# Optimization experiments

Measured on AMD Instinct MI355X. Metric: run time of the kernel, lower is better.

Reference implementation:

```python
import jax, jax.numpy as jnp
import numpy as np

C = 512

def _conv1x1(x, w, b):
    # x: [B, C, T], w: [O, C], b: [O] -> [B, O, T]
    return jnp.einsum('oc,bct->bot', w, x) + b[None, :, None]

def setup_inputs() -> dict:
    key = jax.random.key(0)
    ks = jax.random.split(key, 9)
    B, T = 8, 2048
    s = 1.0 / np.sqrt(C)
    inp = {'x': jax.random.normal(ks[0], (B, C, T), dtype=jnp.float32)}
    names = ['theta', 'phi', 'g', 'w']
    for i, n in enumerate(names):
        inp[f'w_{n}'] = jax.random.uniform(ks[1 + 2 * i], (C, C), jnp.float32, -s, s)
        inp[f'b_{n}'] = jax.random.uniform(ks[2 + 2 * i], (C,), jnp.float32, -s, s)
    return inp

def reference(x, w_theta, b_theta, w_phi, b_phi, w_g, b_g, w_w, b_w):
    relu = jax.nn.relu
    feat_theta = relu(_conv1x1(x, w_theta, b_theta))          # [B, C, T]
    feat_phi = relu(_conv1x1(x, w_phi, b_phi))                # [B, C, T]
    # scores: Q^T K over channel dim -> [B, T, T]
    scores = jnp.einsum('bci,bcj->bij', feat_theta, feat_phi)
    attn = jax.nn.softmax(scores, axis=2)                     # [B, T, T]
    feat_g = relu(_conv1x1(x, w_g, b_g))                      # [B, C, T]
    # attention-weighted V: [B, T, T] x [B, T, C] -> [B, T, C] -> [B, C, T]
    feature = jnp.einsum('bij,bcj->bci', attn, feat_g)
    w_feature = relu(_conv1x1(feature, w_w, b_w))
    return w_feature + x
```

## Files before the change

### kernel.cpp

```cpp
#include <hip/hip_runtime.h>
#include <math.h>

#define C_DIM 512
#define T_DIM 2048
#define B_DIM 8

typedef _Float16 f16;
typedef __attribute__((ext_vector_type(8))) _Float16 half8;
typedef __attribute__((ext_vector_type(4))) _Float16 half4;
typedef __attribute__((ext_vector_type(4))) float floatx4;

__global__ __launch_bounds__(256) void prep_kernel(
    const float* __restrict__ x, f16* __restrict__ xt,
    const float* __restrict__ w0, const float* __restrict__ w1,
    const float* __restrict__ w2, const float* __restrict__ w3,
    f16* __restrict__ o0, f16* __restrict__ o1,
    f16* __restrict__ o2, f16* __restrict__ o3,
    const float* __restrict__ b0, const float* __restrict__ b1,
    float* __restrict__ ob)
{
    __shared__ float xs[32][33];
    const int blk = blockIdx.x;
    const int tid = threadIdx.x;

    if (blk < 1024) {
        const float* src; f16* dst;
        switch (blk >> 8) {
            case 0:  src = w0; dst = o0; break;
            case 1:  src = w1; dst = o1; break;
            case 2:  src = w2; dst = o2; break;
            default: src = w3; dst = o3; break;
        }
        const int idx = ((blk & 255) * 256 + tid) * 4;
        const float4 v = *(const float4*)(src + idx);
        half4 h; h[0] = (f16)v.x; h[1] = (f16)v.y; h[2] = (f16)v.z; h[3] = (f16)v.w;
        *(half4*)(dst + idx) = h;
        return;
    }
    if (blk < 1028) {
        const int i = (blk - 1024) * 256 + tid;
        ob[i] = (i < 512) ? b0[i] : b1[i - 512];
        return;
    }
    {
        const int rr = blk - 1028;
        const int b  = rr >> 10;
        const int rem = rr & 1023;
        const int t0 = (rem & 63) * 32;
        const int c0 = (rem >> 6) * 32;
        const float* xb = x + (size_t)b * C_DIM * T_DIM;
        const int r = tid >> 3, q = tid & 7;

        const float4 v = *(const float4*)(xb + (size_t)(c0 + r) * T_DIM + t0 + q * 4);
        xs[r][q * 4 + 0] = v.x; xs[r][q * 4 + 1] = v.y;
        xs[r][q * 4 + 2] = v.z; xs[r][q * 4 + 3] = v.w;
        __syncthreads();

        f16* xtb = xt + (size_t)b * C_DIM * T_DIM;
        half4 h;
        h[0] = (f16)xs[q * 4 + 0][r]; h[1] = (f16)xs[q * 4 + 1][r];
        h[2] = (f16)xs[q * 4 + 2][r]; h[3] = (f16)xs[q * 4 + 3][r];
        *(half4*)(xtb + (size_t)(t0 + r) * C_DIM + c0 + q * 4) = h;
    }
}

__device__ __forceinline__ void gl16(const f16* g, f16* l)
{
    __builtin_amdgcn_global_load_lds(
        (const __attribute__((address_space(1))) unsigned int*)g,
        (__attribute__((address_space(3))) unsigned int*)l,
        16, 0, 0);
}


template<int MODE>
__global__ __launch_bounds__(512, 2) void gemm256(
    const f16* __restrict__ A, size_t sA, int lda,
    const f16* __restrict__ B, size_t sB, int ldb,
    void* __restrict__ Cp, size_t sC, int ldc,
    const float* __restrict__ bias,
    int gx, int K)
{
    __shared__ __align__(16) f16 As[2][2][256 * 32];
    __shared__ __align__(16) f16 Bs[2][2][256 * 32];

    const int f = blockIdx.x;
    const int bz = f & 7;
    const int flat = f >> 3;
    const int jsc = gx >> 2;
    const int sh = (jsc <= 1) ? 0 : (31 - __builtin_clz(jsc));
    const int s = flat >> 4, rem = flat & 15;
    const int i0 = ((s >> sh) * 4 + (rem >> 2)) * 256;
    const int j0 = (((jsc <= 1) ? 0 : (s & (jsc - 1))) * 4 + (rem & 3)) * 256;

    A += (size_t)bz * sA;
    B += (size_t)bz * sB;

    const int tid  = threadIdx.x;
    const int lane = tid & 63;
    const int wave = tid >> 6;
    const int wy = wave >> 2;
    const int wx = wave & 3;
    const int quad = lane >> 4, l16 = lane & 15;

    const int srow = wave * 32 + (lane >> 2);
    const int sch  = (lane & 3) ^ ((lane >> 3) & 3);
    const f16* gA0 = A + (size_t)(i0 + srow) * lda + sch * 8;
    const f16* gA1 = gA0 + (size_t)16 * lda;
    const f16* gB0 = B + (size_t)(j0 + srow) * ldb + sch * 8;
    const f16* gB1 = gB0 + (size_t)16 * ldb;
    const int wsg = wave * 1024;

    const int xq = (quad ^ ((l16 >> 1) & 3)) << 3;
    const int ra = (wy * 128 + l16) * 32 + xq;
    const int rb = (wx * 64 + l16) * 32 + xq;

    const int nt = K >> 6;

#define STAGE_A(t, q) do {                                                    \
        const int off_ = (t) * 64 + (q) * 32;                                 \
        gl16(gA0 + off_, &As[(t) & 1][q][wsg]);                               \
        gl16(gA1 + off_, &As[(t) & 1][q][wsg + 512]);                         \
    } while (0)
#define STAGE_B(t, q) do {                                                    \
        const int off_ = (t) * 64 + (q) * 32;                                 \
        gl16(gB0 + off_, &Bs[(t) & 1][q][wsg]);                               \
        gl16(gB1 + off_, &Bs[(t) & 1][q][wsg + 512]);                         \
    } while (0)
#define PH_MFMA(B0) do {                                                      \
        __builtin_amdgcn_s_setprio(1);                                        \
        _Pragma("unroll")                                                     \
        for (int mi = 0; mi < 4; ++mi) {                                      \
            _Pragma("unroll")                                                 \
            for (int ni = 0; ni < 4; ++ni)                                    \
                acc[(B0) + mi][ni] = __builtin_amdgcn_mfma_f32_16x16x32_f16(  \
                    af[mi], bf[ni], acc[(B0) + mi][ni], 0, 0, 0);             \
        }                                                                     \
        __builtin_amdgcn_s_setprio(0);                                        \
    } while (0)

    STAGE_A(0, 0); STAGE_B(0, 0);
    STAGE_A(0, 1); STAGE_B(0, 1);
    STAGE_A(1, 0); STAGE_B(1, 0);

    floatx4 acc[8][4] = {};

    for (int t = 0; t < nt; ++t) {
        const f16* sa0 = &As[t & 1][0][0];
        const f16* sb0 = &Bs[t & 1][0][0];
        const f16* sa1 = &As[t & 1][1][0];
        const f16* sb1 = &Bs[t & 1][1][0];
        half8 af[4], bf[4];

        if (t + 1 < nt) asm volatile("s_waitcnt vmcnt(8)\ns_barrier" ::: "memory");
        else            asm volatile("s_waitcnt vmcnt(4)\ns_barrier" ::: "memory");
        #pragma unroll
        for (int ni = 0; ni < 4; ++ni) bf[ni] = *(const half8*)&sb0[rb + ni * 512];
        #pragma unroll
        for (int mi = 0; mi < 4; ++mi) af[mi] = *(const half8*)&sa0[ra + mi * 512];
        if (t + 1 < nt) STAGE_A(t + 1, 1);
        PH_MFMA(0);

        #pragma unroll
        for (int mi = 0; mi < 4; ++mi) af[mi] = *(const half8*)&sa0[ra + 2048 + mi * 512];
        if (t + 1 < nt) STAGE_B(t + 1, 1);
        PH_MFMA(4);

        if (t + 1 < nt) asm volatile("s_waitcnt vmcnt(8)\ns_barrier" ::: "memory");
        else            asm volatile("s_waitcnt vmcnt(0)\ns_barrier" ::: "memory");
        #pragma unroll
        for (int ni = 0; ni < 4; ++ni) bf[ni] = *(const half8*)&sb1[rb + ni * 512];
        #pragma unroll
        for (int mi = 0; mi < 4; ++mi) af[mi] = *(const half8*)&sa1[ra + mi * 512];
        if (t + 2 < nt) STAGE_A(t + 2, 0);
        PH_MFMA(0);

        #pragma unroll
        for (int mi = 0; mi < 4; ++mi) af[mi] = *(const half8*)&sa1[ra + 2048 + mi * 512];
        if (t + 2 < nt) STAGE_B(t + 2, 0);
        PH_MFMA(4);
    }
#undef STAGE_A
#undef STAGE_B
#undef PH_MFMA

    #pragma unroll
    for (int m = 0; m < 8; ++m) {
        #pragma unroll
        for (int ni = 0; ni < 4; ++ni) {
            const int col = j0 + wx * 64 + ni * 16 + l16;
            #pragma unroll
            for (int r = 0; r < 4; ++r) {
                const int row = i0 + wy * 128 + m * 16 + quad * 4 + r;
                float v = acc[m][ni][r];
                if (MODE == 1) { v += bias[col]; v = v > 0.f ? v : 0.f; }
                ((f16*)Cp)[(size_t)bz * sC + (size_t)row * ldc + col] = (f16)v;
            }
        }
    }
}

template<int MODE>
__global__ __launch_bounds__(512, 2) void gemm_wide(
    const f16* __restrict__ A, size_t sA, int lda,
    const f16* __restrict__ B, size_t sB, int ldb,
    void* __restrict__ Cp, size_t sC, int ldc,
    const float* __restrict__ bias,
    const float* __restrict__ resid, size_t sR,
    int gxn, int K)
{
    __shared__ __align__(16) f16 As[2][2][128 * 32];
    __shared__ __align__(16) f16 Bs[2][2][256 * 32];

    const int f = blockIdx.x;
    const int bz = f & 7;
    const int inner = f >> 3;
    const int j0 = (inner % gxn) * 256;
    const int i0 = (inner / gxn) * 128;
    A += (size_t)bz * sA;
    B += (size_t)bz * sB;

    const int tid  = threadIdx.x;
    const int lane = tid & 63;
    const int wave = tid >> 6;
    const int wy = wave >> 2;
    const int wx = wave & 3;
    const int quad = lane >> 4, l16 = lane & 15;

    const int sch = (lane & 3) ^ ((lane >> 3) & 3);
    const f16* gA0 = A + (size_t)(i0 + wave * 16 + (lane >> 2)) * lda + sch * 8;
    const f16* gB0 = B + (size_t)(j0 + wave * 32 + (lane >> 2)) * ldb + sch * 8;
    const f16* gB1 = gB0 + (size_t)16 * ldb;

    const int xq = (quad ^ ((l16 >> 1) & 3)) << 3;
    const int ra = (wy * 64 + l16) * 32 + xq;
    const int rb = (wx * 64 + l16) * 32 + xq;

    const int nt = K >> 6;

#define WSTAGE_A(t, q) do {                                                   \
        gl16(gA0 + (t) * 64 + (q) * 32, &As[(t) & 1][q][wave * 512]);         \
    } while (0)
#define WSTAGE_B(t, q) do {                                                   \
        const int off_ = (t) * 64 + (q) * 32;                                 \
        gl16(gB0 + off_, &Bs[(t) & 1][q][wave * 1024]);                       \
        gl16(gB1 + off_, &Bs[(t) & 1][q][wave * 1024 + 512]);                 \
    } while (0)
#define WPH_MFMA() do {                                                       \
        __builtin_amdgcn_s_setprio(1);                                        \
        _Pragma("unroll")                                                     \
        for (int mi = 0; mi < 4; ++mi) {                                      \
            _Pragma("unroll")                                                 \
            for (int ni = 0; ni < 4; ++ni)                                    \
                acc[mi][ni] = __builtin_amdgcn_mfma_f32_16x16x32_f16(         \
                    af[mi], bf[ni], acc[mi][ni], 0, 0, 0);                    \
        }                                                                     \
        __builtin_amdgcn_s_setprio(0);                                        \
    } while (0)

    WSTAGE_A(0, 0); WSTAGE_B(0, 0);
    WSTAGE_A(0, 1); WSTAGE_B(0, 1);
    WSTAGE_A(1, 0); WSTAGE_B(1, 0);

    floatx4 acc[4][4] = {};

    for (int t = 0; t < nt; ++t) {
        const f16* sa0 = &As[t & 1][0][0];
        const f16* sb0 = &Bs[t & 1][0][0];
        const f16* sa1 = &As[t & 1][1][0];
        const f16* sb1 = &Bs[t & 1][1][0];
        half8 af[4], bf[4];

        if (t + 1 < nt) asm volatile("s_waitcnt vmcnt(6)\ns_barrier" ::: "memory");
        else            asm volatile("s_waitcnt vmcnt(3)\ns_barrier" ::: "memory");
        #pragma unroll
        for (int ni = 0; ni < 4; ++ni) bf[ni] = *(const half8*)&sb0[rb + ni * 512];
        #pragma unroll
        for (int mi = 0; mi < 4; ++mi) af[mi] = *(const half8*)&sa0[ra + mi * 512];
        if (t + 1 < nt) { WSTAGE_A(t + 1, 1); WSTAGE_B(t + 1, 1); }
        WPH_MFMA();

        if (t + 1 < nt) asm volatile("s_waitcnt vmcnt(6)\ns_barrier" ::: "memory");
        else            asm volatile("s_waitcnt vmcnt(0)\ns_barrier" ::: "memory");
        #pragma unroll
        for (int ni = 0; ni < 4; ++ni) bf[ni] = *(const half8*)&sb1[rb + ni * 512];
        #pragma unroll
        for (int mi = 0; mi < 4; ++mi) af[mi] = *(const half8*)&sa1[ra + mi * 512];
        if (t + 2 < nt) { WSTAGE_A(t + 2, 0); WSTAGE_B(t + 2, 0); }
        WPH_MFMA();
    }
#undef WSTAGE_A
#undef WSTAGE_B
#undef WPH_MFMA

    #pragma unroll
    for (int mi = 0; mi < 4; ++mi) {
        #pragma unroll
        for (int ni = 0; ni < 4; ++ni) {
            const int col = j0 + wx * 64 + ni * 16 + l16;
            #pragma unroll
            for (int r = 0; r < 4; ++r) {
                const int row = i0 + wy * 64 + mi * 16 + quad * 4 + r;
                float v = acc[mi][ni][r];
                if (MODE == 2) { v += bias[row]; v = v > 0.f ? v : 0.f; }
                if (MODE == 3) {
                    v += bias[row];
                    v = v > 0.f ? v : 0.f;
                    v += resid[(size_t)bz * sR + (size_t)row * ldc + col];
                    ((float*)Cp)[(size_t)bz * sC + (size_t)row * ldc + col] = v;
                } else {
                    ((f16*)Cp)[(size_t)bz * sC + (size_t)row * ldc + col] = (f16)v;
                }
            }
        }
    }
}

__global__ __launch_bounds__(256) void softmax_f16_kernel(f16* __restrict__ S)
{
    const int lane = threadIdx.x & 63;
    f16* p = S + (size_t)(blockIdx.x * 4 + (threadIdx.x >> 6)) * T_DIM;

    half8 h[4];
    float v[32];
    float m = -1e30f;
    #pragma unroll
    for (int u = 0; u < 4; ++u) {
        h[u] = *((const half8*)p + (u * 64 + lane));
        #pragma unroll
        for (int c = 0; c < 8; ++c) {
            v[u * 8 + c] = (float)h[u][c];
            m = fmaxf(m, v[u * 8 + c]);
        }
    }
    #pragma unroll
    for (int off = 32; off; off >>= 1) m = fmaxf(m, __shfl_xor(m, off));

    float s = 0.f;
    #pragma unroll
    for (int i = 0; i < 32; ++i) { v[i] = __expf(v[i] - m); s += v[i]; }
    #pragma unroll
    for (int off = 32; off; off >>= 1) s += __shfl_xor(s, off);
    const float inv = 1.f / s;

    #pragma unroll
    for (int u = 0; u < 4; ++u) {
        #pragma unroll
        for (int c = 0; c < 8; ++c) h[u][c] = (f16)(v[u * 8 + c] * inv);
        *((half8*)p + (u * 64 + lane)) = h[u];
    }
}

extern "C" void kernel_launch(void* const* d_in, const int* in_sizes, int n_in,
                              void* d_out, int out_size, void* d_ws, size_t ws_size,
                              hipStream_t stream)
{
    const float* x       = (const float*)d_in[0];
    const float* w_theta = (const float*)d_in[1];
    const float* b_theta = (const float*)d_in[2];
    const float* w_phi   = (const float*)d_in[3];
    const float* b_phi   = (const float*)d_in[4];
    const float* w_g     = (const float*)d_in[5];
    const float* b_g     = (const float*)d_in[6];
    const float* w_w     = (const float*)d_in[7];
    const float* b_w     = (const float*)d_in[8];
    float* out = (float*)d_out;

    const size_t FE = (size_t)B_DIM * C_DIM * T_DIM;
    const size_t TC = (size_t)T_DIM * C_DIM;
    const size_t TT = (size_t)T_DIM * T_DIM;

    f16* xt      = (f16*)d_ws;
    f16* wtp     = xt + FE;
    f16* wg_h    = wtp + 524288;
    f16* ww_h    = wg_h + 262144;
    float* btp   = (float*)(ww_h + 262144);
    f16* tp      = (f16*)(btp + 1024);
    f16* g       = tp + (size_t)B_DIM * T_DIM * 1024;
    f16* scores  = g + FE;
    f16* feature = tp;

    const dim3 blk(256);
    const dim3 blk512(512);

    prep_kernel<<<dim3(1024 + 4 + 8192), blk, 0, stream>>>(
        x, xt, w_theta, w_phi, w_g, w_w,
        wtp, wtp + 262144, wg_h, ww_h, b_theta, b_phi, btp);

    gemm256<1><<<dim3(4 * 8 * B_DIM), blk512, 0, stream>>>(
        xt, TC, C_DIM, wtp, 0, C_DIM, tp, (size_t)T_DIM * 1024, 1024,
        btp, 4, C_DIM);
    gemm_wide<2><<<dim3(8 * 4 * B_DIM), blk512, 0, stream>>>(
        wg_h, 0, C_DIM, xt, TC, C_DIM, g, TC, T_DIM, b_g, nullptr, 0,
        8, C_DIM);
    gemm256<0><<<dim3(8 * 8 * B_DIM), blk512, 0, stream>>>(
        tp, (size_t)T_DIM * 1024, 1024, tp + 512, (size_t)T_DIM * 1024, 1024,
        scores, TT, T_DIM, nullptr, 8, C_DIM);
    softmax_f16_kernel<<<dim3(B_DIM * T_DIM / 4), blk, 0, stream>>>(scores);
    gemm_wide<0><<<dim3(2 * 16 * B_DIM), blk512, 0, stream>>>(
        scores, TT, T_DIM, g, TC, T_DIM, feature, TC, C_DIM,
        nullptr, nullptr, 0, 2, T_DIM);
    gemm_wide<3><<<dim3(8 * 4 * B_DIM), blk512, 0, stream>>>(
        ww_h, 0, C_DIM, feature, TC, C_DIM, out, TC, T_DIM, b_w, x, TC,
        8, C_DIM);
}
```

Baseline: 252.3 us.

## Compute two adjacent score tiles per block reusing A rows across tiles

Replaces the scores GEMM with a dual-tile kernel in which each block computes a 256x512 output strip as two consecutive 256x256 tiles, sweeping K twice. The pipelined loads continue straight into the second tile, so there is no separate prologue, and the first tile's accumulators are written out mid-loop. Grid size drops from 512 to 256 blocks, which cuts launch and prologue overhead and keeps the pipeline full across tiles. The cost is fewer blocks for occupancy and a write-out stall in the middle of the K loop.

```diff
diff --git a/kernel.cpp b/kernel.cpp
--- a/kernel.cpp
+++ b/kernel.cpp
@@ -198,6 +198,135 @@
             }
         }
     }
+}
+
+__global__ __launch_bounds__(512, 2) void gemm256_dual(
+    const f16* __restrict__ A, size_t sA, int lda,
+    const f16* __restrict__ B, size_t sB, int ldb,
+    f16* __restrict__ Cp, size_t sC, int ldc,
+    int K)
+{
+    __shared__ __align__(16) f16 As[2][2][256 * 32];
+    __shared__ __align__(16) f16 Bs[2][2][256 * 32];
+
+    const int f = blockIdx.x;
+    const int bz = f & 7;
+    const int inner = f >> 3;
+    const int i0 = (inner >> 2) * 256;
+    const int jb = (inner & 3) * 512;
+
+    A += (size_t)bz * sA;
+    B += (size_t)bz * sB;
+
+    const int tid  = threadIdx.x;
+    const int lane = tid & 63;
+    const int wave = tid >> 6;
+    const int wy = wave >> 2;
+    const int wx = wave & 3;
+    const int quad = lane >> 4, l16 = lane & 15;
+
+    const int srow = wave * 32 + (lane >> 2);
+    const int sch  = (lane & 3) ^ ((lane >> 3) & 3);
+    const f16* gA0 = A + (size_t)(i0 + srow) * lda + sch * 8;
+    const f16* gA1 = gA0 + (size_t)16 * lda;
+    const f16* gB0 = B + (size_t)(jb + srow) * ldb + sch * 8;
+    const f16* gB1 = gB0 + (size_t)16 * ldb;
+    const int wsg = wave * 1024;
+
+    const int xq = (quad ^ ((l16 >> 1) & 3)) << 3;
+    const int ra = (wy * 128 + l16) * 32 + xq;
+    const int rb = (wx * 64 + l16) * 32 + xq;
+
+    const int nt8 = K >> 6;
+    const int ntv = nt8 * 2;
+
+#define DSTAGE_A(t, q) do {                                                   \
+        const int off_ = ((t) & 7) * 64 + (q) * 32;                           \
+        gl16(gA0 + off_, &As[(t) & 1][q][wsg]);                               \
+        gl16(gA1 + off_, &As[(t) & 1][q][wsg + 512]);                         \
+    } while (0)
+#define DSTAGE_B(t, q) do {                                                   \
+        const size_t off_ = (size_t)((t) >> 3) * 256 * ldb                    \
+                          + ((t) & 7) * 64 + (q) * 32;                        \
+        gl16(gB0 + off_, &Bs[(t) & 1][q][wsg]);                               \
+        gl16(gB1 + off_, &Bs[(t) & 1][q][wsg + 512]);                         \
+    } while (0)
+#define PH_MFMA(B0) do {                                                      \
+        __builtin_amdgcn_s_setprio(1);                                        \
+        _Pragma("unroll")                                                     \
+        for (int mi = 0; mi < 4; ++mi) {                                      \
+            _Pragma("unroll")                                                 \
+            for (int ni = 0; ni < 4; ++ni)                                    \
+                acc[(B0) + mi][ni] = __builtin_amdgcn_mfma_f32_16x16x32_f16(  \
+                    af[mi], bf[ni], acc[(B0) + mi][ni], 0, 0, 0);             \
+        }                                                                     \
+        __builtin_amdgcn_s_setprio(0);                                        \
+    } while (0)
+#define DUMP(J0) do {                                                         \
+        _Pragma("unroll")                                                     \
+        for (int m = 0; m < 8; ++m) {                                         \
+            _Pragma("unroll")                                                 \
+            for (int ni = 0; ni < 4; ++ni) {                                  \
+                const int col = (J0) + wx * 64 + ni * 16 + l16;               \
+                _Pragma("unroll")                                             \
+                for (int r = 0; r < 4; ++r) {                                 \
+                    const int row = i0 + wy * 128 + m * 16 + quad * 4 + r;    \
+                    Cp[(size_t)bz * sC + (size_t)row * ldc + col] =           \
+                        (f16)acc[m][ni][r];                                   \
+                    acc[m][ni][r] = 0.f;                                      \
+                }                                                             \
+            }                                                                 \
+        }                                                                     \
+    } while (0)
+
+    DSTAGE_A(0, 0); DSTAGE_B(0, 0);
+    DSTAGE_A(0, 1); DSTAGE_B(0, 1);
+    DSTAGE_A(1, 0); DSTAGE_B(1, 0);
+
+    floatx4 acc[8][4] = {};
+
+    for (int t = 0; t < ntv; ++t) {
+        const f16* sa0 = &As[t & 1][0][0];
+        const f16* sb0 = &Bs[t & 1][0][0];
+        const f16* sa1 = &As[t & 1][1][0];
+        const f16* sb1 = &Bs[t & 1][1][0];
+        half8 af[4], bf[4];
+
+        if (t + 1 < ntv) asm volatile("s_waitcnt vmcnt(8)\ns_barrier" ::: "memory");
+        else             asm volatile("s_waitcnt vmcnt(4)\ns_barrier" ::: "memory");
+        if (t == nt8) DUMP(jb);
+        #pragma unroll
+        for (int ni = 0; ni < 4; ++ni) bf[ni] = *(const half8*)&sb0[rb + ni * 512];
+        #pragma unroll
+        for (int mi = 0; mi < 4; ++mi) af[mi] = *(const half8*)&sa0[ra + mi * 512];
+        if (t + 1 < ntv) DSTAGE_A(t + 1, 1);
+        PH_MFMA(0);
+
+        #pragma unroll
+        for (int mi = 0; mi < 4; ++mi) af[mi] = *(const half8*)&sa0[ra + 2048 + mi * 512];
+        if (t + 1 < ntv) DSTAGE_B(t + 1, 1);
+        PH_MFMA(4);
+
+        if (t + 1 < ntv) asm volatile("s_waitcnt vmcnt(8)\ns_barrier" ::: "memory");
+        else             asm volatile("s_waitcnt vmcnt(0)\ns_barrier" ::: "memory");
+        #pragma unroll
+        for (int ni = 0; ni < 4; ++ni) bf[ni] = *(const half8*)&sb1[rb + ni * 512];
+        #pragma unroll
+        for (int mi = 0; mi < 4; ++mi) af[mi] = *(const half8*)&sa1[ra + mi * 512];
+        if (t + 2 < ntv) DSTAGE_A(t + 2, 0);
+        PH_MFMA(0);
+
+        #pragma unroll
+        for (int mi = 0; mi < 4; ++mi) af[mi] = *(const half8*)&sa1[ra + 2048 + mi * 512];
+        if (t + 2 < ntv) DSTAGE_B(t + 2, 0);
+        PH_MFMA(4);
+    }
+
+    DUMP(jb + 256);
+#undef DSTAGE_A
+#undef DSTAGE_B
+#undef PH_MFMA
+#undef DUMP
 }
 
 template<int MODE>
@@ -393,9 +522,9 @@
     gemm_wide<2><<<dim3(8 * 4 * B_DIM), blk512, 0, stream>>>(
         wg_h, 0, C_DIM, xt, TC, C_DIM, g, TC, T_DIM, b_g, nullptr, 0,
         8, C_DIM);
-    gemm256<0><<<dim3(8 * 8 * B_DIM), blk512, 0, stream>>>(
+    gemm256_dual<<<dim3(256), blk512, 0, stream>>>(
         tp, (size_t)T_DIM * 1024, 1024, tp + 512, (size_t)T_DIM * 1024, 1024,
-        scores, TT, T_DIM, nullptr, 8, C_DIM);
+        scores, TT, T_DIM, C_DIM);
     softmax_f16_kernel<<<dim3(B_DIM * T_DIM / 4), blk, 0, stream>>>(scores);
     gemm_wide<0><<<dim3(2 * 16 * B_DIM), blk512, 0, stream>>>(
         scores, TT, T_DIM, g, TC, T_DIM, feature, TC, C_DIM,
```

New measurement: 262.0 us. 1.04x slower.

## Split gemm256 block tile across 16 waves with 64x64 per-wave tiles

Applied to the files above, without the earlier changes.

Launches gemm256 with 1024 threads (16 waves) instead of 512 and gives each wave a 64x64 sub-tile instead of 128x64. The 256x256 block tile and the double-buffered LDS staging stay, but each wave now issues one global-to-LDS copy per operand per stage, and the vmcnt waits are adjusted to match. The aim is to halve accumulator registers per wave and raise the number of waves available to hide latency. The trade-off is that each MFMA now needs more LDS fragment reads, there are more barriers participants, and the launch_bounds(1024,4) occupancy target may be unreachable or squeeze registers.

```diff
diff --git a/kernel.cpp b/kernel.cpp
--- a/kernel.cpp
+++ b/kernel.cpp
@@ -74,7 +74,7 @@
 
 
 template<int MODE>
-__global__ __launch_bounds__(512, 2) void gemm256(
+__global__ __launch_bounds__(1024, 4) void gemm256(
     const f16* __restrict__ A, size_t sA, int lda,
     const f16* __restrict__ B, size_t sB, int ldb,
     void* __restrict__ Cp, size_t sC, int ldc,
@@ -103,47 +103,38 @@
     const int wx = wave & 3;
     const int quad = lane >> 4, l16 = lane & 15;
 
-    const int srow = wave * 32 + (lane >> 2);
+    const int srow = wave * 16 + (lane >> 2);
     const int sch  = (lane & 3) ^ ((lane >> 3) & 3);
     const f16* gA0 = A + (size_t)(i0 + srow) * lda + sch * 8;
-    const f16* gA1 = gA0 + (size_t)16 * lda;
     const f16* gB0 = B + (size_t)(j0 + srow) * ldb + sch * 8;
-    const f16* gB1 = gB0 + (size_t)16 * ldb;
-    const int wsg = wave * 1024;
+    const int wsg = wave * 512;
 
     const int xq = (quad ^ ((l16 >> 1) & 3)) << 3;
-    const int ra = (wy * 128 + l16) * 32 + xq;
+    const int ra = (wy * 64 + l16) * 32 + xq;
     const int rb = (wx * 64 + l16) * 32 + xq;
 
     const int nt = K >> 6;
 
-#define STAGE_A(t, q) do {                                                    \
+#define STAGE(t, q) do {                                                      \
         const int off_ = (t) * 64 + (q) * 32;                                 \
         gl16(gA0 + off_, &As[(t) & 1][q][wsg]);                               \
-        gl16(gA1 + off_, &As[(t) & 1][q][wsg + 512]);                         \
-    } while (0)
-#define STAGE_B(t, q) do {                                                    \
-        const int off_ = (t) * 64 + (q) * 32;                                 \
         gl16(gB0 + off_, &Bs[(t) & 1][q][wsg]);                               \
-        gl16(gB1 + off_, &Bs[(t) & 1][q][wsg + 512]);                         \
-    } while (0)
-#define PH_MFMA(B0) do {                                                      \
+    } while (0)
+#define PH_MFMA() do {                                                        \
         __builtin_amdgcn_s_setprio(1);                                        \
         _Pragma("unroll")                                                     \
         for (int mi = 0; mi < 4; ++mi) {                                      \
             _Pragma("unroll")                                                 \
             for (int ni = 0; ni < 4; ++ni)                                    \
-                acc[(B0) + mi][ni] = __builtin_amdgcn_mfma_f32_16x16x32_f16(  \
-                    af[mi], bf[ni], acc[(B0) + mi][ni], 0, 0, 0);             \
+                acc[mi][ni] = __builtin_amdgcn_mfma_f32_16x16x32_f16(         \
+                    af[mi], bf[ni], acc[mi][ni], 0, 0, 0);                    \
         }                                                                     \
         __builtin_amdgcn_s_setprio(0);                                        \
     } while (0)
 
-    STAGE_A(0, 0); STAGE_B(0, 0);
-    STAGE_A(0, 1); STAGE_B(0, 1);
-    STAGE_A(1, 0); STAGE_B(1, 0);
-
-    floatx4 acc[8][4] = {};
+    STAGE(0, 0); STAGE(0, 1); STAGE(1, 0);
+
+    floatx4 acc[4][4] = {};
 
     for (int t = 0; t < nt; ++t) {
         const f16* sa0 = &As[t & 1][0][0];
@@ -152,47 +143,36 @@
         const f16* sb1 = &Bs[t & 1][1][0];
         half8 af[4], bf[4];
 
-        if (t + 1 < nt) asm volatile("s_waitcnt vmcnt(8)\ns_barrier" ::: "memory");
-        else            asm volatile("s_waitcnt vmcnt(4)\ns_barrier" ::: "memory");
+        if (t + 1 < nt) asm volatile("s_waitcnt vmcnt(4)\ns_barrier" ::: "memory");
+        else            asm volatile("s_waitcnt vmcnt(2)\ns_barrier" ::: "memory");
         #pragma unroll
         for (int ni = 0; ni < 4; ++ni) bf[ni] = *(const half8*)&sb0[rb + ni * 512];
         #pragma unroll
         for (int mi = 0; mi < 4; ++mi) af[mi] = *(const half8*)&sa0[ra + mi * 512];
-        if (t + 1 < nt) STAGE_A(t + 1, 1);
-        PH_MFMA(0);
-
-        #pragma unroll
-        for (int mi = 0; mi < 4; ++mi) af[mi] = *(const half8*)&sa0[ra + 2048 + mi * 512];
-        if (t + 1 < nt) STAGE_B(t + 1, 1);
-        PH_MFMA(4);
-
-        if (t + 1 < nt) asm volatile("s_waitcnt vmcnt(8)\ns_barrier" ::: "memory");
+        if (t + 1 < nt) STAGE(t + 1, 1);
+        PH_MFMA();
+
+        if (t + 1 < nt) asm volatile("s_waitcnt vmcnt(4)\ns_barrier" ::: "memory");
         else            asm volatile("s_waitcnt vmcnt(0)\ns_barrier" ::: "memory");
         #pragma unroll
         for (int ni = 0; ni < 4; ++ni) bf[ni] = *(const half8*)&sb1[rb + ni * 512];
         #pragma unroll
         for (int mi = 0; mi < 4; ++mi) af[mi] = *(const half8*)&sa1[ra + mi * 512];
-        if (t + 2 < nt) STAGE_A(t + 2, 0);
-        PH_MFMA(0);
-
-        #pragma unroll
-        for (int mi = 0; mi < 4; ++mi) af[mi] = *(const half8*)&sa1[ra + 2048 + mi * 512];
-        if (t + 2 < nt) STAGE_B(t + 2, 0);
-        PH_MFMA(4);
-    }
-#undef STAGE_A
-#undef STAGE_B
+        if (t + 2 < nt) STAGE(t + 2, 0);
+        PH_MFMA();
+    }
+#undef STAGE
 #undef PH_MFMA
 
     #pragma unroll
-    for (int m = 0; m < 8; ++m) {
+    for (int mi = 0; mi < 4; ++mi) {
         #pragma unroll
         for (int ni = 0; ni < 4; ++ni) {
             const int col = j0 + wx * 64 + ni * 16 + l16;
             #pragma unroll
             for (int r = 0; r < 4; ++r) {
-                const int row = i0 + wy * 128 + m * 16 + quad * 4 + r;
-                float v = acc[m][ni][r];
+                const int row = i0 + wy * 64 + mi * 16 + quad * 4 + r;
+                float v = acc[mi][ni][r];
                 if (MODE == 1) { v += bias[col]; v = v > 0.f ? v : 0.f; }
                 ((f16*)Cp)[(size_t)bz * sC + (size_t)row * ldc + col] = (f16)v;
             }
@@ -382,18 +362,19 @@
 
     const dim3 blk(256);
     const dim3 blk512(512);
+    const dim3 blk1024(1024);
 
     prep_kernel<<<dim3(1024 + 4 + 8192), blk, 0, stream>>>(
         x, xt, w_theta, w_phi, w_g, w_w,
         wtp, wtp + 262144, wg_h, ww_h, b_theta, b_phi, btp);
 
-    gemm256<1><<<dim3(4 * 8 * B_DIM), blk512, 0, stream>>>(
+    gemm256<1><<<dim3(4 * 8 * B_DIM), blk1024, 0, stream>>>(
         xt, TC, C_DIM, wtp, 0, C_DIM, tp, (size_t)T_DIM * 1024, 1024,
         btp, 4, C_DIM);
     gemm_wide<2><<<dim3(8 * 4 * B_DIM), blk512, 0, stream>>>(
         wg_h, 0, C_DIM, xt, TC, C_DIM, g, TC, T_DIM, b_g, nullptr, 0,
         8, C_DIM);
-    gemm256<0><<<dim3(8 * 8 * B_DIM), blk512, 0, stream>>>(
+    gemm256<0><<<dim3(8 * 8 * B_DIM), blk1024, 0, stream>>>(
         tp, (size_t)T_DIM * 1024, 1024, tp + 512, (size_t)T_DIM * 1024, 1024,
         scores, TT, T_DIM, nullptr, 8, C_DIM);
     softmax_f16_kernel<<<dim3(B_DIM * T_DIM / 4), blk, 0, stream>>>(scores);
```

New measurement: 255.5 us. No clear change (+1.3%).
